# Kernel tuning notes

Measured on AMD Instinct MI355X. Metric: run time of the kernel, lower is better.

## Reference

```python
import jax, jax.numpy as jnp
import numpy as np

N_NODES = 10000
N_EDGES = 640000
IN_DIM = 128
OUT_DIM = 128


def setup_inputs() -> dict:
    key = jax.random.key(0)
    k1, k2, k3, k4, k5 = jax.random.split(key, 5)
    h = jax.random.normal(k1, (N_NODES, IN_DIM), dtype=jnp.float32)
    src = jax.random.randint(k2, (N_EDGES,), 0, N_NODES, dtype=jnp.int32)
    dst = jax.random.randint(k3, (N_EDGES,), 0, N_NODES, dtype=jnp.int32)
    # nn.Linear default init: U(-1/sqrt(fan_in), 1/sqrt(fan_in)); scale normals similarly
    W_fc = jax.random.normal(k4, (OUT_DIM, IN_DIM), dtype=jnp.float32) / np.sqrt(IN_DIM)
    W_attn = jax.random.normal(k5, (1, 2 * OUT_DIM), dtype=jnp.float32) / np.sqrt(2 * OUT_DIM)
    return {"h": h, "src": src, "dst": dst, "W_fc": W_fc, "W_attn": W_attn}


def reference(h, src, dst, W_fc, W_attn):
    n = h.shape[0]
    # z = fc(h)
    z = h @ W_fc.T                                   # [N, out]
    # edge attention: attn_fc(cat([z_src, z_dst])) == z_src @ a_s + z_dst @ a_d
    a_src = W_attn[0, :OUT_DIM]                      # [out]
    a_dst = W_attn[0, OUT_DIM:]                      # [out]
    e = z @ a_src                                    # [N] per-node src contribution
    f = z @ a_dst                                    # [N] per-node dst contribution
    score = e[src] + f[dst]                          # [E] edge logits
    # segment softmax over incoming edges of each dst node
    m = jax.ops.segment_max(score, dst, num_segments=n)   # [N]
    m = jnp.where(jnp.isfinite(m), m, 0.0)                # guard empty segments
    ex = jnp.exp(score - m[dst])                           # [E]
    den = jax.ops.segment_sum(ex, dst, num_segments=n)     # [N]
    alpha = ex / jnp.where(den > 0, den, 1.0)[dst]          # [E]
    # weighted scatter-sum of source z into dst
    msg = alpha[:, None] * z[src]                           # [E, out]
    h_out = jax.ops.segment_sum(msg, dst, num_segments=n)  # [N, out]
    return h_out
```

## Files before the change

kernel.cpp:

```cpp
#include <hip/hip_runtime.h>

#define NN 10000
#define NE 640000
#define DIM 128
#define HNB 64
#define HEPB 10000
#define FCN 64
#define FCB ((NN + FCN - 1) / FCN)
#define DEGCAP 512
#define PAD 128

static __device__ __forceinline__ unsigned short f2bf(float f) {
    unsigned u = __float_as_uint(f);
    unsigned r = (u + 0x7FFFu + ((u >> 16) & 1u)) >> 16;
    return (unsigned short)r;
}
static __device__ __forceinline__ float bfhi(unsigned u) { return __uint_as_float(u & 0xFFFF0000u); }
static __device__ __forceinline__ float bflo(unsigned u) { return __uint_as_float(u << 16); }

__global__ __launch_bounds__(512) void histT_kernel(
    const int* __restrict__ dst, int* __restrict__ bh,
    const float* __restrict__ W, float* __restrict__ Wt)
{
    __shared__ int lh[NN];
    const int b = blockIdx.x, t = threadIdx.x;
    for (int v = t; v < NN; v += 512) lh[v] = 0;
    if (t < 256) {
        int idx = b * 256 + t;
        Wt[(idx & 127) * DIM + (idx >> 7)] = W[idx];
    }
    __syncthreads();
    const int4* d4 = (const int4*)(dst + b * HEPB);
    for (int i = t; i < HEPB / 4; i += 512) {
        int4 d = d4[i];
        atomicAdd(&lh[d.x], 1); atomicAdd(&lh[d.y], 1);
        atomicAdd(&lh[d.z], 1); atomicAdd(&lh[d.w], 1);
    }
    __syncthreads();
    for (int v = t; v < NN; v += 512) bh[(size_t)b * NN + v] = lh[v];
}

__global__ __launch_bounds__(512) void colscan_kernel(
    int* __restrict__ bh, int* __restrict__ cnt)
{
    const int lane = threadIdx.x & 63, w = threadIdx.x >> 6;
    const int v = blockIdx.x * 8 + w;
    int c = bh[(size_t)lane * NN + v];
    int x = c;
    #pragma unroll
    for (int o = 1; o <= 32; o <<= 1) {
        int y = __shfl_up(x, o, 64);
        if (lane >= o) x += y;
    }
    bh[(size_t)lane * NN + v] = x - c;
    if (lane == 63) cnt[v] = x;
}

__global__ __launch_bounds__(512, 2) void scatfc_kernel(
    const int* __restrict__ src, const int* __restrict__ dst,
    const int* __restrict__ base, int* __restrict__ esrc,
    const float* __restrict__ h, const float* __restrict__ Wt,
    const float* __restrict__ Wa, unsigned short* __restrict__ zb,
    float* __restrict__ e)
{
    __shared__ int smem[10240];
    const int bid = blockIdx.x, t = threadIdx.x;

    if (bid < HNB) {
        int* lcur = smem;
        for (int v = t; v < NN; v += 512) lcur[v] = 0;
        __syncthreads();
        const int4* d4 = (const int4*)(dst + bid * HEPB);
        const int4* s4 = (const int4*)(src + bid * HEPB);
        const int* brow = base + (size_t)bid * NN;
        for (int i = t; i < HEPB / 4; i += 512) {
            int4 d = d4[i]; int4 s = s4[i];
            int r;
            r = brow[d.x] + atomicAdd(&lcur[d.x], 1); if (r < PAD) esrc[(d.x << 7) + r] = s.x;
            r = brow[d.y] + atomicAdd(&lcur[d.y], 1); if (r < PAD) esrc[(d.y << 7) + r] = s.y;
            r = brow[d.z] + atomicAdd(&lcur[d.z], 1); if (r < PAD) esrc[(d.z << 7) + r] = s.z;
            r = brow[d.w] + atomicAdd(&lcur[d.w], 1); if (r < PAD) esrc[(d.w << 7) + r] = s.w;
        }
    } else {
        float* hs = (float*)smem;
        const int jl = t & 31, jq = jl * 4;
        const int ng = t >> 5;
        const int i0 = (bid - HNB) * FCN;

        const float4* h4 = (const float4*)h;
        float4* hs4 = (float4*)hs;
        for (int u = t; u < FCN * 32; u += 512) {
            int gi = i0 + (u >> 5);
            hs4[u] = (gi < NN) ? h4[(size_t)gi * 32 + (u & 31)]
                               : make_float4(0.f, 0.f, 0.f, 0.f);
        }
        __syncthreads();

        float acc[4][4] = {};
        for (int k = 0; k < DIM; k += 4) {
            float4 wv[4];
            #pragma unroll
            for (int kk = 0; kk < 4; ++kk)
                wv[kk] = *(const float4*)&Wt[(k + kk) * DIM + jq];
            const float* wf = (const float*)wv;
            #pragma unroll
            for (int m = 0; m < 4; ++m) {
                float4 hv = *(const float4*)&hs[(4 * ng + m) * DIM + k];
                float hvf[4] = {hv.x, hv.y, hv.z, hv.w};
                #pragma unroll
                for (int kk = 0; kk < 4; ++kk)
                    #pragma unroll
                    for (int jm = 0; jm < 4; ++jm)
                        acc[m][jm] += hvf[kk] * wf[kk * 4 + jm];
            }
        }

        const float a0 = Wa[jq], a1 = Wa[jq + 1], a2 = Wa[jq + 2], a3 = Wa[jq + 3];
        #pragma unroll
        for (int m = 0; m < 4; ++m) {
            int gi = i0 + 4 * ng + m;
            float ep = acc[m][0] * a0 + acc[m][1] * a1 + acc[m][2] * a2 + acc[m][3] * a3;
            #pragma unroll
            for (int o = 16; o > 0; o >>= 1) ep += __shfl_xor(ep, o, 64);
            if (gi < NN) {
                ushort4 zo;
                zo.x = f2bf(acc[m][0]); zo.y = f2bf(acc[m][1]);
                zo.z = f2bf(acc[m][2]); zo.w = f2bf(acc[m][3]);
                *(ushort4*)&zb[(size_t)gi * DIM + jq] = zo;
                if (jl == 0) e[gi] = ep;
            }
        }
    }
}

__global__ __launch_bounds__(64) void agg64_kernel(
    const int* __restrict__ cnt, const int* __restrict__ esrc,
    const float* __restrict__ e, const unsigned* __restrict__ zb32,
    float* __restrict__ out)
{
    __shared__ int   es[DEGCAP];
    __shared__ float ew[DEGCAP];
    const int v = blockIdx.x, t = threadIdx.x;
    const int beg = v << 7;
    int deg = cnt[v];
    if (deg > PAD) deg = PAD;

    float lm = -3.4e38f;
    for (int i = t; i < deg; i += 64) {
        int s = esrc[beg + i];
        float ev = e[s];
        es[i] = s; ew[i] = ev;
        lm = fmaxf(lm, ev);
    }
    #pragma unroll
    for (int o = 32; o > 0; o >>= 1) lm = fmaxf(lm, __shfl_xor(lm, o, 64));

    float ls = 0.f;
    for (int i = t; i < deg; i += 64) {
        float w = __expf(ew[i] - lm);
        ew[i] = w; ls += w;
    }
    #pragma unroll
    for (int o = 32; o > 0; o >>= 1) ls += __shfl_xor(ls, o, 64);
    const float inv = (ls > 0.f) ? (1.f / ls) : 0.f;
    __syncthreads();

    float a0 = 0.f, a1 = 0.f, a2 = 0.f, a3 = 0.f;
    int i = 0;
    for (; i + 3 < deg; i += 4) {
        unsigned u0 = zb32[(size_t)es[i]     * 64 + t];
        unsigned u1 = zb32[(size_t)es[i + 1] * 64 + t];
        unsigned u2 = zb32[(size_t)es[i + 2] * 64 + t];
        unsigned u3 = zb32[(size_t)es[i + 3] * 64 + t];
        a0 += ew[i]     * bflo(u0); a1 += ew[i]     * bfhi(u0);
        a2 += ew[i + 1] * bflo(u1); a3 += ew[i + 1] * bfhi(u1);
        a0 += ew[i + 2] * bflo(u2); a1 += ew[i + 2] * bfhi(u2);
        a2 += ew[i + 3] * bflo(u3); a3 += ew[i + 3] * bfhi(u3);
    }
    for (; i < deg; ++i) {
        unsigned u = zb32[(size_t)es[i] * 64 + t];
        a0 += ew[i] * bflo(u); a1 += ew[i] * bfhi(u);
    }
    float2 r;
    r.x = (a0 + a2) * inv;
    r.y = (a1 + a3) * inv;
    *(float2*)&out[(size_t)v * DIM + 2 * t] = r;
}

extern "C" void kernel_launch(void* const* d_in, const int* in_sizes, int n_in,
                              void* d_out, int out_size, void* d_ws, size_t ws_size,
                              hipStream_t stream)
{
    const float* h     = (const float*)d_in[0];
    const int*   src   = (const int*)d_in[1];
    const int*   dst   = (const int*)d_in[2];
    const float* Wfc   = (const float*)d_in[3];
    const float* Wattn = (const float*)d_in[4];
    float* out = (float*)d_out;

    unsigned short* zb   = (unsigned short*)d_ws;
    float*          e    = (float*)(zb + (size_t)NN * DIM + 16);
    int*            cnt  = (int*)(e + 10016);
    float*          Wt   = (float*)(cnt + 10016);
    int*            bh   = (int*)(Wt + 16384);
    int*            esrc = bh + (size_t)HNB * NN;

    histT_kernel<<<HNB, 512, 0, stream>>>(dst, bh, Wfc, Wt);
    colscan_kernel<<<NN / 8, 512, 0, stream>>>(bh, cnt);
    scatfc_kernel<<<HNB + FCB, 512, 0, stream>>>(src, dst, bh, esrc,
                                                 h, Wt, Wattn, zb, e);
    agg64_kernel<<<NN, 64, 0, stream>>>(cnt, esrc, e, (const unsigned*)zb, out);
}
```

Before: 56.26 us.

## Pack four destination nodes per block and split edges across half-waves

The aggregation kernel now runs four wavefronts per 256-thread block, one destination node each, with per-wave shared buffers, so the block-wide barrier is gone. Inside each wave the two 32-lane halves take alternating edges and load 8-byte uint2 chunks of the bf16 rows, then combine their partial sums with a cross-half shuffle and write one float4 per lane. This aims to cut block-launch overhead and put more gather loads in flight per wave. The cost is an extra shuffle reduction, and half the lanes sit idle during the store.

Result: no change. 55.80 us (-0.8%).

```diff
diff --git a/kernel.cpp b/kernel.cpp
--- a/kernel.cpp
+++ b/kernel.cpp
@@ -7,7 +7,6 @@
 #define HEPB 10000
 #define FCN 64
 #define FCB ((NN + FCN - 1) / FCN)
-#define DEGCAP 512
 #define PAD 128
 
 static __device__ __forceinline__ unsigned short f2bf(float f) {
@@ -133,58 +132,82 @@
     }
 }
 
-__global__ __launch_bounds__(64) void agg64_kernel(
+__global__ __launch_bounds__(256) void agg_kernel(
     const int* __restrict__ cnt, const int* __restrict__ esrc,
     const float* __restrict__ e, const unsigned* __restrict__ zb32,
     float* __restrict__ out)
 {
-    __shared__ int   es[DEGCAP];
-    __shared__ float ew[DEGCAP];
-    const int v = blockIdx.x, t = threadIdx.x;
+    __shared__ int   es[4][PAD];
+    __shared__ float ew[4][PAD];
+    const int w = threadIdx.x >> 6, lane = threadIdx.x & 63;
+    const int v = blockIdx.x * 4 + w;
+    if (v >= NN) return;
+    int* esw = es[w];
+    float* eww = ew[w];
     const int beg = v << 7;
     int deg = cnt[v];
     if (deg > PAD) deg = PAD;
 
     float lm = -3.4e38f;
-    for (int i = t; i < deg; i += 64) {
-        int s = esrc[beg + i];
-        float ev = e[s];
-        es[i] = s; ew[i] = ev;
-        lm = fmaxf(lm, ev);
+    #pragma unroll
+    for (int i = lane; i < PAD; i += 64) {
+        if (i < deg) {
+            int s = esrc[beg + i];
+            float ev = e[s];
+            esw[i] = s; eww[i] = ev;
+            lm = fmaxf(lm, ev);
+        }
     }
     #pragma unroll
     for (int o = 32; o > 0; o >>= 1) lm = fmaxf(lm, __shfl_xor(lm, o, 64));
 
     float ls = 0.f;
-    for (int i = t; i < deg; i += 64) {
-        float w = __expf(ew[i] - lm);
-        ew[i] = w; ls += w;
+    #pragma unroll
+    for (int i = lane; i < PAD; i += 64) {
+        if (i < deg) {
+            float p = __expf(eww[i] - lm);
+            eww[i] = p; ls += p;
+        }
     }
     #pragma unroll
     for (int o = 32; o > 0; o >>= 1) ls += __shfl_xor(ls, o, 64);
     const float inv = (ls > 0.f) ? (1.f / ls) : 0.f;
-    __syncthreads();
-
+
+    const uint2* zb2 = (const uint2*)zb32;
+    const int half = lane >> 5, hl = lane & 31;
     float a0 = 0.f, a1 = 0.f, a2 = 0.f, a3 = 0.f;
-    int i = 0;
-    for (; i + 3 < deg; i += 4) {
-        unsigned u0 = zb32[(size_t)es[i]     * 64 + t];
-        unsigned u1 = zb32[(size_t)es[i + 1] * 64 + t];
-        unsigned u2 = zb32[(size_t)es[i + 2] * 64 + t];
-        unsigned u3 = zb32[(size_t)es[i + 3] * 64 + t];
-        a0 += ew[i]     * bflo(u0); a1 += ew[i]     * bfhi(u0);
-        a2 += ew[i + 1] * bflo(u1); a3 += ew[i + 1] * bfhi(u1);
-        a0 += ew[i + 2] * bflo(u2); a1 += ew[i + 2] * bfhi(u2);
-        a2 += ew[i + 3] * bflo(u3); a3 += ew[i + 3] * bfhi(u3);
-    }
-    for (; i < deg; ++i) {
-        unsigned u = zb32[(size_t)es[i] * 64 + t];
-        a0 += ew[i] * bflo(u); a1 += ew[i] * bfhi(u);
-    }
-    float2 r;
-    r.x = (a0 + a2) * inv;
-    r.y = (a1 + a3) * inv;
-    *(float2*)&out[(size_t)v * DIM + 2 * t] = r;
+    int i = half;
+    for (; i + 6 < deg; i += 8) {
+        int   s0 = esw[i],  s1 = esw[i + 2],  s2 = esw[i + 4],  s3 = esw[i + 6];
+        float w0 = eww[i],  w1 = eww[i + 2],  w2 = eww[i + 4],  w3 = eww[i + 6];
+        uint2 u0 = zb2[(size_t)s0 * 32 + hl];
+        uint2 u1 = zb2[(size_t)s1 * 32 + hl];
+        uint2 u2 = zb2[(size_t)s2 * 32 + hl];
+        uint2 u3 = zb2[(size_t)s3 * 32 + hl];
+        a0 += w0 * bflo(u0.x); a1 += w0 * bfhi(u0.x);
+        a2 += w0 * bflo(u0.y); a3 += w0 * bfhi(u0.y);
+        a0 += w1 * bflo(u1.x); a1 += w1 * bfhi(u1.x);
+        a2 += w1 * bflo(u1.y); a3 += w1 * bfhi(u1.y);
+        a0 += w2 * bflo(u2.x); a1 += w2 * bfhi(u2.x);
+        a2 += w2 * bflo(u2.y); a3 += w2 * bfhi(u2.y);
+        a0 += w3 * bflo(u3.x); a1 += w3 * bfhi(u3.x);
+        a2 += w3 * bflo(u3.y); a3 += w3 * bfhi(u3.y);
+    }
+    for (; i < deg; i += 2) {
+        int s = esw[i]; float p = eww[i];
+        uint2 u = zb2[(size_t)s * 32 + hl];
+        a0 += p * bflo(u.x); a1 += p * bfhi(u.x);
+        a2 += p * bflo(u.y); a3 += p * bfhi(u.y);
+    }
+    a0 += __shfl_xor(a0, 32, 64);
+    a1 += __shfl_xor(a1, 32, 64);
+    a2 += __shfl_xor(a2, 32, 64);
+    a3 += __shfl_xor(a3, 32, 64);
+    if (half == 0) {
+        float4 r;
+        r.x = a0 * inv; r.y = a1 * inv; r.z = a2 * inv; r.w = a3 * inv;
+        *(float4*)&out[(size_t)v * DIM + 4 * hl] = r;
+    }
 }
 
 extern "C" void kernel_launch(void* const* d_in, const int* in_sizes, int n_in,
@@ -209,5 +232,5 @@
     colscan_kernel<<<NN / 8, 512, 0, stream>>>(bh, cnt);
     scatfc_kernel<<<HNB + FCB, 512, 0, stream>>>(src, dst, bh, esrc,
                                                  h, Wt, Wattn, zb, e);
-    agg64_kernel<<<NN, 64, 0, stream>>>(cnt, esrc, e, (const unsigned*)zb, out);
-}
+    agg_kernel<<<(NN + 3) / 4, 256, 0, stream>>>(cnt, esrc, e, (const unsigned*)zb, out);
+}
```
